# Optimization experiments

Hardware: AMD Instinct MI355X
Metric: run time of the kernel (lower is better)

The kernel has to match this reference:

```python
import jax, jax.numpy as jnp
import numpy as np

N, E, D, L = 50000, 600000, 128, 2  # nodes, edges, hidden_dim, num_gnn_layers
NEG_SLOPE = 0.2  # PyG GATv2Conv default negative_slope


def setup_inputs() -> dict:
    key = jax.random.key(0)
    ks = jax.random.split(key, 10)
    s = 1.0 / np.sqrt(D)
    return {
        "x": jax.random.normal(ks[0], (N, D), jnp.float32),
        "edge_index": jax.random.randint(ks[1], (2, E), 0, N, dtype=jnp.int32),
        # per-layer GATv2 params (stacked over L layers)
        "Wl": jax.random.normal(ks[2], (L, D, D), jnp.float32) * s,  # lin_l (source)
        "bl": jnp.zeros((L, D), jnp.float32),
        "Wr": jax.random.normal(ks[3], (L, D, D), jnp.float32) * s,  # lin_r (target)
        "br": jnp.zeros((L, D), jnp.float32),
        "att": jax.random.normal(ks[4], (L, D), jnp.float32) * s,
        "bias": jnp.zeros((L, D), jnp.float32),
        # shared residual Linear
        "W_res": jax.random.normal(ks[5], (D, D), jnp.float32) * s,
        "b_res": jnp.zeros((D,), jnp.float32),
    }


def reference(x, edge_index, Wl, bl, Wr, br, att, bias, W_res, b_res):
    n = x.shape[0]
    # add self loops (PyG GATv2Conv default add_self_loops=True)
    loops = jnp.arange(n, dtype=edge_index.dtype)
    src = jnp.concatenate([edge_index[0], loops])  # source j (messages)
    dst = jnp.concatenate([edge_index[1], loops])  # target i (aggregation)

    def conv(h, i):
        xl = h @ Wl[i] + bl[i]  # [N, D] source transform
        xr = h @ Wr[i] + br[i]  # [N, D] target transform
        m = xl[src] + xr[dst]   # [E+N, D] gathered edge messages
        e = jnp.einsum('ed,d->e', jnp.where(m > 0, m, NEG_SLOPE * m), att[i])
        # segment softmax over incoming edges of each destination node
        emax = jax.lax.stop_gradient(jax.ops.segment_max(e, dst, num_segments=n))
        ex = jnp.exp(e - emax[dst])
        denom = jax.ops.segment_sum(ex, dst, num_segments=n)
        alpha = ex / (denom[dst] + 1e-16)
        out = jax.ops.segment_sum(alpha[:, None] * xl[src], dst, num_segments=n)
        return out + bias[i]

    for i in range(Wl.shape[0]):
        x = jax.nn.relu(conv(x, i) + x @ W_res + b_res)
    return x
```

## Files before the change

### kernel.cpp

```cpp
#include <hip/hip_runtime.h>
#include <math.h>


#define DIM 128
#define NEG_SLOPE 0.2f
#define TPW 4

typedef __attribute__((ext_vector_type(8))) short short8;
typedef __attribute__((ext_vector_type(4))) float floatx4;
typedef __attribute__((ext_vector_type(2))) float f32x2;

static __device__ __forceinline__ unsigned short f2b(float f) {
    unsigned u = __float_as_uint(f);
    unsigned r = (u + 0x7FFFu + ((u >> 16) & 1u)) >> 16;
    return (unsigned short)r;
}
static __device__ __forceinline__ f32x2 cvt2(unsigned u) {
    f32x2 r;
    r.x = __uint_as_float(u << 16);
    r.y = __uint_as_float(u & 0xffff0000u);
    return r;
}
static __device__ __forceinline__ f32x2 abs2(f32x2 a) {
    f32x2 r;
    r.x = __builtin_fabsf(a.x);
    r.y = __builtin_fabsf(a.y);
    return r;
}

__global__ void k_count(const int* __restrict__ dst, int E, int* __restrict__ counts) {
    int k = blockIdx.x * blockDim.x + threadIdx.x;
    if (k < E) atomicAdd(&counts[dst[k]], 1);
}

__global__ void k_scan1(const int* __restrict__ counts, int n,
                        int* __restrict__ rowptr, int* __restrict__ bsum) {
    __shared__ int s[256];
    int tid = threadIdx.x;
    int i = blockIdx.x * 256 + tid;
    int v = (i < n) ? (counts[i] + 1) : 0;
    s[tid] = v;
    __syncthreads();
    for (int off = 1; off < 256; off <<= 1) {
        int t = (tid >= off) ? s[tid - off] : 0;
        __syncthreads();
        s[tid] += t;
        __syncthreads();
    }
    if (i < n) rowptr[i + 1] = s[tid];
    if (tid == 255) bsum[blockIdx.x] = s[255];
}

__global__ void k_scan3(int* __restrict__ rowptr, const int* __restrict__ bsum,
                        int n, int* __restrict__ counts_to_cursors, int nb) {
    __shared__ int s[256];
    int tid = threadIdx.x;
    int v = (tid < nb) ? bsum[tid] : 0;
    s[tid] = v;
    __syncthreads();
    for (int off = 1; off < 256; off <<= 1) {
        int t = (tid >= off) ? s[tid - off] : 0;
        __syncthreads();
        s[tid] += t;
        __syncthreads();
    }
    int add = (blockIdx.x > 0) ? s[blockIdx.x - 1] : 0;
    int i = blockIdx.x * 256 + tid;
    if (i < n) {
        int cnt = counts_to_cursors[i] + 1;
        int vv = rowptr[i + 1] + add;
        rowptr[i + 1] = vv;
        counts_to_cursors[i] = vv - cnt;
    }
    if (i == 0) rowptr[0] = 0;
}

__global__ void k_scatter(const int* __restrict__ src, const int* __restrict__ dst,
                          int E, int n, int* __restrict__ cur, int* __restrict__ srt) {
    int k = blockIdx.x * blockDim.x + threadIdx.x;
    int tot = E + n;
    if (k >= tot) return;
    int s, d;
    if (k < E) { s = src[k]; d = dst[k]; }
    else       { s = k - E;  d = s; }
    int p = atomicAdd(&cur[d], 1);
    srt[p] = s;
}

__global__ void k_pre(const float* __restrict__ Wl, const float* __restrict__ Wr,
                      const float* __restrict__ Wres, unsigned short* __restrict__ wfrag,
                      const float* __restrict__ h, unsigned short* __restrict__ hfrag,
                      int* __restrict__ tmpc, int n, int ntiles) {
    int blk = blockIdx.x;
    if (blk < 48) {
        int idx = blk * 256 + threadIdx.x;
        int lane = idx & 63;
        int nr   = (idx >> 6) & 7;
        int ks   = (idx >> 9) & 3;
        int v    = idx >> 11;
        int sec = v % 3, l = v / 3;
        const float* W = (sec == 0) ? (Wl + l * DIM * DIM)
                       : (sec == 1) ? (Wr + l * DIM * DIM) : Wres;
        int nn = nr * 16 + (lane & 15);
        int k0 = ks * 32 + ((lane >> 4) << 3);
        ushort4 a, b;
        a.x = f2b(W[(k0 + 0) * DIM + nn]); a.y = f2b(W[(k0 + 1) * DIM + nn]);
        a.z = f2b(W[(k0 + 2) * DIM + nn]); a.w = f2b(W[(k0 + 3) * DIM + nn]);
        b.x = f2b(W[(k0 + 4) * DIM + nn]); b.y = f2b(W[(k0 + 5) * DIM + nn]);
        b.z = f2b(W[(k0 + 6) * DIM + nn]); b.w = f2b(W[(k0 + 7) * DIM + nn]);
        *(ushort4*)(wfrag + (size_t)idx * 8) = a;
        *(ushort4*)(wfrag + (size_t)idx * 8 + 4) = b;
    } else if (blk < 48 + ntiles) {
        int idx = (blk - 48) * 256 + threadIdx.x;
        int lane = idx & 63;
        int ks   = (idx >> 6) & 3;
        int tile = idx >> 8;
        int row  = tile * 16 + (lane & 15);
        int col0 = ks * 32 + ((lane >> 4) << 3);
        ushort4 a = {0, 0, 0, 0}, b = {0, 0, 0, 0};
        if (row < n) {
            float4 v0 = *(const float4*)(h + (size_t)row * DIM + col0);
            float4 v1 = *(const float4*)(h + (size_t)row * DIM + col0 + 4);
            a.x = f2b(v0.x); a.y = f2b(v0.y); a.z = f2b(v0.z); a.w = f2b(v0.w);
            b.x = f2b(v1.x); b.y = f2b(v1.y); b.z = f2b(v1.z); b.w = f2b(v1.w);
        }
        *(ushort4*)(hfrag + (size_t)idx * 8) = a;
        *(ushort4*)(hfrag + (size_t)idx * 8 + 4) = b;
    } else {
        int i = (blk - 48 - ntiles) * 256 + threadIdx.x;
        if (i < n) tmpc[i] = 0;
    }
}

__global__ __launch_bounds__(256, 2) void k_gemm(
    const unsigned short* __restrict__ hfrag, const unsigned short* __restrict__ wfrag,
    const float* __restrict__ bl, const float* __restrict__ br, const float* __restrict__ bres,
    unsigned short* __restrict__ XLb, unsigned short* __restrict__ XRb,
    unsigned short* __restrict__ RESb, int ntiles)
{
    int sec  = blockIdx.y;
    int lane = threadIdx.x & 63;
    int w    = threadIdx.x >> 6;

    const unsigned short* wbase = wfrag + (size_t)sec * (4 * 8 * 64 * 8);
    short8 bf[4][8];
#pragma unroll
    for (int ks = 0; ks < 4; ks++)
#pragma unroll
        for (int nr = 0; nr < 8; nr++)
            bf[ks][nr] = *(const short8*)(wbase + (((ks * 8 + nr) * 64 + lane) << 3));

    const float* bias = (sec == 0) ? bl : (sec == 1) ? br : bres;
    unsigned short* C = (sec == 0) ? XLb : (sec == 1) ? XRb : RESb;
    int colb = (lane >> 4) << 2;
    float4 bv[8];
#pragma unroll
    for (int nr = 0; nr < 8; nr++) bv[nr] = *(const float4*)(bias + nr * 16 + colb);

    int wid = blockIdx.x * 4 + w;
#pragma unroll
    for (int i = 0; i < TPW; i++) {
        int t = wid * TPW + i;
        if (t >= ntiles) break;
        short8 a[4];
#pragma unroll
        for (int ks = 0; ks < 4; ks++)
            a[ks] = *(const short8*)(hfrag + (((t * 4 + ks) * 64 + lane) << 3));
        floatx4 acc[8];
#pragma unroll
        for (int nr = 0; nr < 8; nr++) acc[nr] = (floatx4){0.f, 0.f, 0.f, 0.f};
#pragma unroll
        for (int ks = 0; ks < 4; ks++)
#pragma unroll
            for (int nr = 0; nr < 8; nr++)
                acc[nr] = __builtin_amdgcn_mfma_f32_16x16x32_bf16(bf[ks][nr], a[ks], acc[nr], 0, 0, 0);

        int row = t * 16 + (lane & 15);
        size_t rb = (size_t)row * DIM;
#pragma unroll
        for (int nr = 0; nr < 8; nr++) {
            ushort4 u;
            u.x = f2b(acc[nr][0] + bv[nr].x);
            u.y = f2b(acc[nr][1] + bv[nr].y);
            u.z = f2b(acc[nr][2] + bv[nr].z);
            u.w = f2b(acc[nr][3] + bv[nr].w);
            *(ushort4*)(C + rb + nr * 16 + colb) = u;
        }
    }
}

#define EDGE_P(K)                                                        \
    f32x2 v01_##K = cvt2(e##K.x), v23_##K = cvt2(e##K.y);                \
    float p##K;                                                          \
    {                                                                    \
        f32x2 t01 = v01_##K + x01;                                       \
        f32x2 t23 = v23_##K + x23;                                       \
        f32x2 pp = a6_01 * t01 + a4_01 * abs2(t01);                      \
        pp += a6_23 * t23;                                               \
        pp += a4_23 * abs2(t23);                                         \
        p##K = pp.x + pp.y;                                              \
    }

__global__ __launch_bounds__(256, 8) void k_aggr(
    const unsigned short* __restrict__ XLb, const unsigned short* __restrict__ XRb,
    const unsigned short* __restrict__ RESb, const float* __restrict__ att,
    const float* __restrict__ bias, const int* __restrict__ rowptr,
    const int* __restrict__ srt, float* __restrict__ outF,
    unsigned short* __restrict__ fragOut, int writeFrag, int n)
{
    int wave = threadIdx.x >> 6;
    int lane = threadIdx.x & 63;
    int half = lane >> 5, sl = lane & 31;
    int node = blockIdx.x * 8 + wave * 2 + half;
    bool valid = node < n;
    int nclamp = valid ? node : (n - 1);
    int d0 = sl << 2;

    const float S6 = 0.6f * 1.44269504089f;
    const float S4 = 0.4f * 1.44269504089f;
    float4 af = *(const float4*)(att + d0);
    f32x2 a6_01 = {S6 * af.x, S6 * af.y}, a6_23 = {S6 * af.z, S6 * af.w};
    f32x2 a4_01 = {S4 * af.x, S4 * af.y}, a4_23 = {S4 * af.z, S4 * af.w};

    uint2 xru = *(const uint2*)(XRb + (size_t)nclamp * DIM + d0);
    f32x2 x01 = cvt2(xru.x), x23 = cvt2(xru.y);

    int beg = rowptr[nclamp], end = valid ? rowptr[nclamp + 1] : beg;

    const uint2* R = (const uint2*)XLb;

    f32x2 acc01 = {0.f, 0.f}, acc23 = {0.f, 0.f};
    float den = 0.f;

    for (int j = beg; j < end; j += 4) {
        int j1 = (j + 1 < end) ? j + 1 : j;
        int j2 = (j + 2 < end) ? j + 2 : j;
        int j3 = (j + 3 < end) ? j + 3 : j;
        int s0 = srt[j], s1 = srt[j1], s2 = srt[j2], s3 = srt[j3];
        uint2 e0 = R[(size_t)s0 * 32 + sl];
        uint2 e1 = R[(size_t)s1 * 32 + sl];
        uint2 e2 = R[(size_t)s2 * 32 + sl];
        uint2 e3 = R[(size_t)s3 * 32 + sl];
        EDGE_P(0) EDGE_P(1) EDGE_P(2) EDGE_P(3)
#pragma unroll
        for (int off = 16; off >= 1; off >>= 1) {
            p0 += __shfl_xor(p0, off);
            p1 += __shfl_xor(p1, off);
            p2 += __shfl_xor(p2, off);
            p3 += __shfl_xor(p3, off);
        }
        float w0 = __builtin_exp2f(fminf(p0, 120.f));
        float w1 = (j + 1 < end) ? __builtin_exp2f(fminf(p1, 120.f)) : 0.f;
        float w2 = (j + 2 < end) ? __builtin_exp2f(fminf(p2, 120.f)) : 0.f;
        float w3 = (j + 3 < end) ? __builtin_exp2f(fminf(p3, 120.f)) : 0.f;
        den += (w0 + w1) + (w2 + w3);
        acc01 += w0 * v01_0 + w1 * v01_1;
        acc23 += w0 * v23_0 + w1 * v23_1;
        acc01 += w2 * v01_2 + w3 * v01_3;
        acc23 += w2 * v23_2 + w3 * v23_3;
    }

    if (!valid) return;

    float inv = 1.f / (den + 1e-16f);
    uint2 ru = *(const uint2*)(RESb + (size_t)node * DIM + d0);
    f32x2 r01 = cvt2(ru.x), r23 = cvt2(ru.y);
    float4 b4 = *(const float4*)(bias + d0);
    float4 o;
    o.x = fmaxf(acc01.x * inv + b4.x + r01.x, 0.f);
    o.y = fmaxf(acc01.y * inv + b4.y + r01.y, 0.f);
    o.z = fmaxf(acc23.x * inv + b4.z + r23.x, 0.f);
    o.w = fmaxf(acc23.y * inv + b4.w + r23.y, 0.f);

    if (writeFrag) {
        int tile = node >> 4;
        int ks = sl >> 3;
        int li = (node & 15) + (((sl >> 1) & 3) << 4);
        int j0 = (sl & 1) << 2;
        ushort4 u;
        u.x = f2b(o.x); u.y = f2b(o.y); u.z = f2b(o.z); u.w = f2b(o.w);
        *(ushort4*)(fragOut + ((size_t)((tile * 4 + ks) * 64 + li) << 3) + j0) = u;
    } else {
        *(float4*)(outF + (size_t)node * DIM + d0) = o;
    }
}

extern "C" void kernel_launch(void* const* d_in, const int* in_sizes, int n_in,
                              void* d_out, int out_size, void* d_ws, size_t ws_size,
                              hipStream_t stream) {
    const float* x    = (const float*)d_in[0];
    const int*   ei   = (const int*)d_in[1];
    const float* Wl   = (const float*)d_in[2];
    const float* bl   = (const float*)d_in[3];
    const float* Wr   = (const float*)d_in[4];
    const float* br   = (const float*)d_in[5];
    const float* att  = (const float*)d_in[6];
    const float* bias = (const float*)d_in[7];
    const float* Wres = (const float*)d_in[8];
    const float* bres = (const float*)d_in[9];

    int n = in_sizes[0] / DIM;
    int E = in_sizes[1] / 2;
    int ntiles = (n + 15) >> 4;
    const int* srcIdx = ei;
    const int* dstIdx = ei + E;

    unsigned short* xlb   = (unsigned short*)d_ws;
    unsigned short* xrb   = xlb + (size_t)n * DIM;
    unsigned short* resb  = xrb + (size_t)n * DIM;
    unsigned short* hfrag = resb + (size_t)n * DIM;
    unsigned short* wfrag = hfrag + (size_t)ntiles * 16 * DIM;
    int* rowptr = (int*)(wfrag + 2 * 3 * DIM * DIM);
    int* tmpc   = rowptr + (n + 1);
    int* srt    = tmpc + n;
    int* bsum   = srt + (E + n + 8);

    int nb1 = (n + 255) / 256;

    k_pre<<<48 + ntiles + nb1, 256, 0, stream>>>(Wl, Wr, Wres, wfrag, x, hfrag,
                                                 tmpc, n, ntiles);
    k_count<<<(E + 255) / 256, 256, 0, stream>>>(dstIdx, E, tmpc);
    k_scan1<<<nb1, 256, 0, stream>>>(tmpc, n, rowptr, bsum);
    k_scan3<<<nb1, 256, 0, stream>>>(rowptr, bsum, n, tmpc, nb1);
    k_scatter<<<(E + n + 255) / 256, 256, 0, stream>>>(srcIdx, dstIdx, E, n, tmpc, srt);

    int gx = (ntiles + 4 * TPW - 1) / (4 * TPW);
    for (int l = 0; l < 2; l++) {
        dim3 g(gx, 3);
        k_gemm<<<g, 256, 0, stream>>>(hfrag, wfrag + (size_t)l * 3 * 4 * 8 * 64 * 8,
                                      bl + (size_t)l * DIM, br + (size_t)l * DIM, bres,
                                      xlb, xrb, resb, ntiles);
        k_aggr<<<(n + 7) / 8, 256, 0, stream>>>(xlb, xrb, resb, att + (size_t)l * DIM,
                                                bias + (size_t)l * DIM, rowptr, srt,
                                                (float*)d_out, hfrag, (l == 0) ? 1 : 0, n);
    }
}
```

Measured before the change: 202.9 us.

## Sort nodes by in-degree bins to balance aggregation work across waves

```diff
diff --git a/kernel.cpp b/kernel.cpp
--- a/kernel.cpp
+++ b/kernel.cpp
@@ -5,6 +5,7 @@
 #define DIM 128
 #define NEG_SLOPE 0.2f
 #define TPW 4
+#define NBIN 64
 
 typedef __attribute__((ext_vector_type(8))) short short8;
 typedef __attribute__((ext_vector_type(4))) float floatx4;
@@ -34,13 +35,20 @@
 }
 
 __global__ void k_scan1(const int* __restrict__ counts, int n,
-                        int* __restrict__ rowptr, int* __restrict__ bsum) {
+                        int* __restrict__ rowptr, int* __restrict__ bsum,
+                        int* __restrict__ hist) {
     __shared__ int s[256];
+    __shared__ int hb[NBIN];
     int tid = threadIdx.x;
+    if (tid < NBIN) hb[tid] = 0;
     int i = blockIdx.x * 256 + tid;
     int v = (i < n) ? (counts[i] + 1) : 0;
     s[tid] = v;
     __syncthreads();
+    if (i < n) {
+        int bin = v < NBIN ? v : NBIN - 1;
+        atomicAdd(&hb[bin], 1);
+    }
     for (int off = 1; off < 256; off <<= 1) {
         int t = (tid >= off) ? s[tid - off] : 0;
         __syncthreads();
@@ -49,10 +57,13 @@
     }
     if (i < n) rowptr[i + 1] = s[tid];
     if (tid == 255) bsum[blockIdx.x] = s[255];
+    __syncthreads();
+    if (tid < NBIN && hb[tid]) atomicAdd(&hist[tid], hb[tid]);
 }
 
 __global__ void k_scan3(int* __restrict__ rowptr, const int* __restrict__ bsum,
-                        int n, int* __restrict__ counts_to_cursors, int nb) {
+                        int n, int* __restrict__ counts_to_cursors, int nb,
+                        const int* __restrict__ hist, int* __restrict__ bcur) {
     __shared__ int s[256];
     int tid = threadIdx.x;
     int v = (tid < nb) ? bsum[tid] : 0;
@@ -73,18 +84,42 @@
         counts_to_cursors[i] = vv - cnt;
     }
     if (i == 0) rowptr[0] = 0;
+
+    if (blockIdx.x == 0) {
+        __syncthreads();
+        int hv = (tid < NBIN) ? hist[tid] : 0;
+        s[tid] = hv;
+        __syncthreads();
+        for (int off = 1; off < NBIN; off <<= 1) {
+            int t = (tid + off < NBIN) ? s[tid + off] : 0;
+            __syncthreads();
+            if (tid < NBIN) s[tid] += t;
+            __syncthreads();
+        }
+        if (tid < NBIN) bcur[tid] = s[tid] - hv;
+    }
 }
 
 __global__ void k_scatter(const int* __restrict__ src, const int* __restrict__ dst,
-                          int E, int n, int* __restrict__ cur, int* __restrict__ srt) {
+                          int E, int n, int* __restrict__ cur, int* __restrict__ srt,
+                          const int* __restrict__ rowptr, int* __restrict__ bcur,
+                          int* __restrict__ nodeord) {
     int k = blockIdx.x * blockDim.x + threadIdx.x;
-    int tot = E + n;
-    if (k >= tot) return;
-    int s, d;
-    if (k < E) { s = src[k]; d = dst[k]; }
-    else       { s = k - E;  d = s; }
-    int p = atomicAdd(&cur[d], 1);
-    srt[p] = s;
+    if (k < E) {
+        int s = src[k], d = dst[k];
+        int p = atomicAdd(&cur[d], 1);
+        srt[p] = s;
+    } else if (k < E + n) {
+        int s = k - E;
+        int p = atomicAdd(&cur[s], 1);
+        srt[p] = s;
+    } else if (k < E + 2 * n) {
+        int i = k - E - n;
+        int deg = rowptr[i + 1] - rowptr[i];
+        int bin = deg < NBIN ? deg : NBIN - 1;
+        int pos = atomicAdd(&bcur[bin], 1);
+        nodeord[pos] = i;
+    }
 }
 
 __global__ void k_pre(const float* __restrict__ Wl, const float* __restrict__ Wr,
@@ -128,7 +163,7 @@
         *(ushort4*)(hfrag + (size_t)idx * 8 + 4) = b;
     } else {
         int i = (blk - 48 - ntiles) * 256 + threadIdx.x;
-        if (i < n) tmpc[i] = 0;
+        if (i < n + 2 * NBIN) tmpc[i] = 0;
     }
 }
 
@@ -205,15 +240,16 @@
     const unsigned short* __restrict__ XLb, const unsigned short* __restrict__ XRb,
     const unsigned short* __restrict__ RESb, const float* __restrict__ att,
     const float* __restrict__ bias, const int* __restrict__ rowptr,
-    const int* __restrict__ srt, float* __restrict__ outF,
-    unsigned short* __restrict__ fragOut, int writeFrag, int n)
+    const int* __restrict__ srt, const int* __restrict__ nodeord,
+    float* __restrict__ outF, unsigned short* __restrict__ fragOut,
+    int writeFrag, int n)
 {
     int wave = threadIdx.x >> 6;
     int lane = threadIdx.x & 63;
     int half = lane >> 5, sl = lane & 31;
-    int node = blockIdx.x * 8 + wave * 2 + half;
-    bool valid = node < n;
-    int nclamp = valid ? node : (n - 1);
+    int gid = blockIdx.x * 8 + wave * 2 + half;
+    bool valid = gid < n;
+    int node = nodeord[valid ? gid : (n - 1)];
     int d0 = sl << 2;
 
     const float S6 = 0.6f * 1.44269504089f;
@@ -222,10 +258,10 @@
     f32x2 a6_01 = {S6 * af.x, S6 * af.y}, a6_23 = {S6 * af.z, S6 * af.w};
     f32x2 a4_01 = {S4 * af.x, S4 * af.y}, a4_23 = {S4 * af.z, S4 * af.w};
 
-    uint2 xru = *(const uint2*)(XRb + (size_t)nclamp * DIM + d0);
+    uint2 xru = *(const uint2*)(XRb + (size_t)node * DIM + d0);
     f32x2 x01 = cvt2(xru.x), x23 = cvt2(xru.y);
 
-    int beg = rowptr[nclamp], end = valid ? rowptr[nclamp + 1] : beg;
+    int beg = rowptr[node], end = valid ? rowptr[node + 1] : beg;
 
     const uint2* R = (const uint2*)XLb;
 
@@ -310,19 +346,25 @@
     unsigned short* resb  = xrb + (size_t)n * DIM;
     unsigned short* hfrag = resb + (size_t)n * DIM;
     unsigned short* wfrag = hfrag + (size_t)ntiles * 16 * DIM;
-    int* rowptr = (int*)(wfrag + 2 * 3 * DIM * DIM);
-    int* tmpc   = rowptr + (n + 1);
-    int* srt    = tmpc + n;
-    int* bsum   = srt + (E + n + 8);
+    int* rowptr  = (int*)(wfrag + 2 * 3 * DIM * DIM);
+    int* tmpc    = rowptr + (n + 1);
+    int* hist    = tmpc + n;
+    int* bcur    = hist + NBIN;
+    int* nodeord = bcur + NBIN;
+    int* srt     = nodeord + n;
+    int* bsum    = srt + (E + n + 8);
 
     int nb1 = (n + 255) / 256;
-
-    k_pre<<<48 + ntiles + nb1, 256, 0, stream>>>(Wl, Wr, Wres, wfrag, x, hfrag,
+    int nbz = (n + 2 * NBIN + 255) / 256;
+
+    k_pre<<<48 + ntiles + nbz, 256, 0, stream>>>(Wl, Wr, Wres, wfrag, x, hfrag,
                                                  tmpc, n, ntiles);
     k_count<<<(E + 255) / 256, 256, 0, stream>>>(dstIdx, E, tmpc);
-    k_scan1<<<nb1, 256, 0, stream>>>(tmpc, n, rowptr, bsum);
-    k_scan3<<<nb1, 256, 0, stream>>>(rowptr, bsum, n, tmpc, nb1);
-    k_scatter<<<(E + n + 255) / 256, 256, 0, stream>>>(srcIdx, dstIdx, E, n, tmpc, srt);
+    k_scan1<<<nb1, 256, 0, stream>>>(tmpc, n, rowptr, bsum, hist);
+    k_scan3<<<nb1, 256, 0, stream>>>(rowptr, bsum, n, tmpc, nb1, hist, bcur);
+    k_scatter<<<(E + 2 * n + 255) / 256, 256, 0, stream>>>(srcIdx, dstIdx, E, n,
+                                                           tmpc, srt, rowptr,
+                                                           bcur, nodeord);
 
     int gx = (ntiles + 4 * TPW - 1) / (4 * TPW);
     for (int l = 0; l < 2; l++) {
@@ -332,6 +374,7 @@
                                       xlb, xrb, resb, ntiles);
         k_aggr<<<(n + 7) / 8, 256, 0, stream>>>(xlb, xrb, resb, att + (size_t)l * DIM,
                                                 bias + (size_t)l * DIM, rowptr, srt,
-                                                (float*)d_out, hfrag, (l == 0) ? 1 : 0, n);
-    }
-}
+                                                nodeord, (float*)d_out, hfrag,
+                                                (l == 0) ? 1 : 0, n);
+    }
+}
```

Measured after the change: 338.0 us. +66.6%, slower.
